# Performance work log

Measured on AMD Instinct MI355X. Metric: run time of the kernel, lower is better.

## Reference

```python
import jax, jax.numpy as jnp
import numpy as np


def softmax_one(x, axis=-1):
    # off-by-one softmax: exp(x - max) / (1 + sum(exp(x - max)))
    x = x - jnp.max(x, axis=axis, keepdims=True)
    exp_x = jnp.exp(x)
    return exp_x / (1.0 + jnp.sum(exp_x, axis=axis, keepdims=True))


def setup_inputs() -> dict:
    key = jax.random.key(0)
    kq, kk, kv = jax.random.split(key, 3)
    B, H, S, D = 2, 16, 2048, 64
    q = jax.random.normal(kq, (B, H, S, D), dtype=jnp.float32)
    k = jax.random.normal(kk, (B, H, S, D), dtype=jnp.float32)
    v = jax.random.normal(kv, (B, H, S, D), dtype=jnp.float32)
    return {"q": q, "k": k, "v": v}


def reference(q, k, v):
    d_k = k.shape[-1]
    scale = 1.0 / jnp.sqrt(jnp.asarray(d_k, dtype=q.dtype))
    # scores: [B, H, Sq, Sk]
    scores = jnp.einsum("bhqd,bhkd->bhqk", q, k) * scale
    p_attn = softmax_one(scores, axis=-1)
    # dropout p=0.0 -> identity
    out = jnp.einsum("bhqk,bhkd->bhqd", p_attn, v)
    return (out, p_attn)
```

## Files before the change

kernel.cpp:

```cpp
#include <hip/hip_runtime.h>

#define ATTN_S  2048
#define ATTN_D  64
#define ATTN_BH 32
#define QT      128
#define KT      64
#define NWAVE   8
#define LOG2E   1.4426950408889634f

typedef _Float16 half8 __attribute__((ext_vector_type(8)));
typedef _Float16 half4v __attribute__((ext_vector_type(4)));
typedef _Float16 half2v __attribute__((ext_vector_type(2)));
typedef float    floatx4 __attribute__((ext_vector_type(4)));

static __device__ __forceinline__ float fast_exp2(float x) {
#if __has_builtin(__builtin_amdgcn_exp2f)
  return __builtin_amdgcn_exp2f(x);
#else
  return exp2f(x);
#endif
}

__global__ __launch_bounds__(512)
void attn_softmax1_kernel(const float* __restrict__ Q,
                          const float* __restrict__ K,
                          const float* __restrict__ V,
                          float* __restrict__ Out,
                          float* __restrict__ P)
{
  __shared__ _Float16 sK[KT][72];
  __shared__ _Float16 sV[ATTN_D][72];
  __shared__ float    sP[NWAVE][16][68];

  const int tid  = threadIdx.x;
  const int w    = tid >> 6;
  const int lane = tid & 63;
  const int quad = lane >> 4;
  const int l15  = lane & 15;

  const int bh = blockIdx.x >> 4;
  const int q0 = (blockIdx.x & 15) * QT;

  const float* Qb = Q + (size_t)bh * ATTN_S * ATTN_D;
  const float* Kb = K + (size_t)bh * ATTN_S * ATTN_D;
  const float* Vb = V + (size_t)bh * ATTN_S * ATTN_D;
  float*       Ob = Out + (size_t)bh * ATTN_S * ATTN_D;
  float*       Pb = P + (size_t)bh * (size_t)ATTN_S * ATTN_S;

  const int qrow = q0 + w * 16 + l15;
  half8 aq[2];
  {
    const float* qr = Qb + (size_t)qrow * ATTN_D;
#pragma unroll
    for (int ch = 0; ch < 2; ++ch) {
      const floatx4* qv = (const floatx4*)(qr + ch * 32 + quad * 8);
      floatx4 f0 = qv[0], f1 = qv[1];
#pragma unroll
      for (int j = 0; j < 4; ++j) {
        aq[ch][j]     = (_Float16)(f0[j] * 0.125f);
        aq[ch][4 + j] = (_Float16)(f1[j] * 0.125f);
      }
    }
  }

  float mrow[4], lrow[4];
#pragma unroll
  for (int r = 0; r < 4; ++r) { mrow[r] = -3.0e38f; lrow[r] = 0.0f; }

#pragma unroll 1
  for (int kt = 0; kt < ATTN_S; kt += KT) {
    __syncthreads();
#pragma unroll
    for (int i = 0; i < 2; ++i) {
      int idx = tid + 512 * i;
      int r = idx >> 4, c4 = idx & 15;
      floatx4 f = *(const floatx4*)(Kb + (size_t)(kt + r) * ATTN_D + c4 * 4);
      half4v h = { (_Float16)f[0], (_Float16)f[1], (_Float16)f[2], (_Float16)f[3] };
      *(half4v*)&sK[r][c4 * 4] = h;
    }
    __syncthreads();

#pragma unroll
    for (int n = 0; n < 4; ++n) {
      half8 bk0 = *(const half8*)&sK[n * 16 + l15][quad * 8];
      half8 bk1 = *(const half8*)&sK[n * 16 + l15][32 + quad * 8];
      floatx4 acc = {0.f, 0.f, 0.f, 0.f};
      acc = __builtin_amdgcn_mfma_f32_16x16x32_f16(aq[0], bk0, acc, 0, 0, 0);
      acc = __builtin_amdgcn_mfma_f32_16x16x32_f16(aq[1], bk1, acc, 0, 0, 0);
#pragma unroll
      for (int r = 0; r < 4; ++r) {
        float s = acc[r];
        mrow[r] = fmaxf(mrow[r], s);
        lrow[r] += fast_exp2(s * LOG2E);
      }
    }
  }

  float rrow[4];
#pragma unroll
  for (int r = 0; r < 4; ++r) {
    float m = mrow[r], l = lrow[r];
#pragma unroll
    for (int off = 1; off < 16; off <<= 1) {
      m = fmaxf(m, __shfl_xor(m, off, 64));
      l += __shfl_xor(l, off, 64);
    }
    rrow[r] = 1.0f / (fast_exp2(m * LOG2E) + l);
  }

  floatx4 oacc[4];
#pragma unroll
  for (int d = 0; d < 4; ++d) oacc[d] = (floatx4){0.f, 0.f, 0.f, 0.f};

#pragma unroll 1
  for (int kt = 0; kt < ATTN_S; kt += KT) {
    __syncthreads();
#pragma unroll
    for (int i = 0; i < 2; ++i) {
      int idx = tid + 512 * i;
      int r = idx >> 4, c4 = idx & 15;
      floatx4 f = *(const floatx4*)(Kb + (size_t)(kt + r) * ATTN_D + c4 * 4);
      half4v h = { (_Float16)f[0], (_Float16)f[1], (_Float16)f[2], (_Float16)f[3] };
      *(half4v*)&sK[r][c4 * 4] = h;
    }
    {
      int rp = tid >> 4, c4 = tid & 15;
      floatx4 f0 = *(const floatx4*)(Vb + (size_t)(kt + 2 * rp) * ATTN_D + c4 * 4);
      floatx4 f1 = *(const floatx4*)(Vb + (size_t)(kt + 2 * rp + 1) * ATTN_D + c4 * 4);
#pragma unroll
      for (int c = 0; c < 4; ++c) {
        half2v h = { (_Float16)f0[c], (_Float16)f1[c] };
        *(half2v*)&sV[c4 * 4 + c][2 * rp] = h;
      }
    }
    __syncthreads();

#pragma unroll
    for (int n = 0; n < 4; ++n) {
      half8 bk0 = *(const half8*)&sK[n * 16 + l15][quad * 8];
      half8 bk1 = *(const half8*)&sK[n * 16 + l15][32 + quad * 8];
      floatx4 acc = {0.f, 0.f, 0.f, 0.f};
      acc = __builtin_amdgcn_mfma_f32_16x16x32_f16(aq[0], bk0, acc, 0, 0, 0);
      acc = __builtin_amdgcn_mfma_f32_16x16x32_f16(aq[1], bk1, acc, 0, 0, 0);
#pragma unroll
      for (int r = 0; r < 4; ++r) {
        float p = fast_exp2(acc[r] * LOG2E) * rrow[r];
        sP[w][quad * 4 + r][n * 16 + l15] = p;
      }
    }
#pragma unroll
    for (int ch = 0; ch < 2; ++ch) {
      const float* prow = &sP[w][l15][ch * 32 + quad * 8];
      half8 ap;
#pragma unroll
      for (int j = 0; j < 8; ++j) ap[j] = (_Float16)prow[j];
#pragma unroll
      for (int ds = 0; ds < 4; ++ds) {
        half8 bv = *(const half8*)&sV[ds * 16 + l15][ch * 32 + quad * 8];
        oacc[ds] = __builtin_amdgcn_mfma_f32_16x16x32_f16(ap, bv, oacc[ds], 0, 0, 0);
      }
    }
    {
      const int growbase = q0 + w * 16;
#pragma unroll
      for (int i = 0; i < 4; ++i) {
        int r = i * 4 + quad;
        floatx4 val = *(const floatx4*)&sP[w][r][l15 * 4];
        *(floatx4*)(Pb + (size_t)(growbase + r) * ATTN_S + kt + l15 * 4) = val;
      }
    }
  }

  {
    const int grow = q0 + w * 16 + quad * 4;
#pragma unroll
    for (int ds = 0; ds < 4; ++ds)
#pragma unroll
      for (int r = 0; r < 4; ++r)
        Ob[(size_t)(grow + r) * ATTN_D + ds * 16 + l15] = oacc[ds][r];
  }
}

extern "C" void kernel_launch(void* const* d_in, const int* in_sizes, int n_in,
                              void* d_out, int out_size, void* d_ws, size_t ws_size,
                              hipStream_t stream) {
  const float* Q = (const float*)d_in[0];
  const float* K = (const float*)d_in[1];
  const float* V = (const float*)d_in[2];
  float* Out = (float*)d_out;
  float* P   = Out + (size_t)ATTN_BH * ATTN_S * ATTN_D;

  dim3 grid(ATTN_BH * (ATTN_S / QT));
  dim3 block(512);
  attn_softmax1_kernel<<<grid, block, 0, stream>>>(Q, K, V, Out, P);
}
```

Before: 675.5 us.

## Preconvert Q/K/V to fp16 workspace and double-buffer tiles via direct LDS loads

A separate pre-pass converts Q (pre-scaled), K (XOR-swizzled) and V (transposed and swizzled) to fp16 in the workspace. The attention kernel then streams K/V tiles with global_load_lds into double-buffered LDS, overlapping the next tile's load with compute. It also swaps MFMA operand order so each lane holds a whole query row, which removes the shuffle reductions and lets P be written straight from registers instead of staging it through LDS. The cost is an extra kernel launch, workspace traffic, and a dependence on a large enough workspace.

Result: no change. 667.9 us (-1.1%).

```diff
diff --git a/kernel.cpp b/kernel.cpp
--- a/kernel.cpp
+++ b/kernel.cpp
@@ -1,17 +1,20 @@
 #include <hip/hip_runtime.h>
+#include <stdint.h>
 
 #define ATTN_S  2048
 #define ATTN_D  64
 #define ATTN_BH 32
 #define QT      128
 #define KT      64
+#define NT      (ATTN_S / KT)
 #define NWAVE   8
 #define LOG2E   1.4426950408889634f
 
-typedef _Float16 half8 __attribute__((ext_vector_type(8)));
-typedef _Float16 half4v __attribute__((ext_vector_type(4)));
-typedef _Float16 half2v __attribute__((ext_vector_type(2)));
+typedef _Float16 half8   __attribute__((ext_vector_type(8)));
+typedef _Float16 half4v  __attribute__((ext_vector_type(4)));
 typedef float    floatx4 __attribute__((ext_vector_type(4)));
+
+#define QH_ELEMS ((size_t)ATTN_BH * ATTN_S * ATTN_D)
 
 static __device__ __forceinline__ float fast_exp2(float x) {
 #if __has_builtin(__builtin_amdgcn_exp2f)
@@ -21,176 +24,196 @@
 #endif
 }
 
-__global__ __launch_bounds__(512)
-void attn_softmax1_kernel(const float* __restrict__ Q,
-                          const float* __restrict__ K,
-                          const float* __restrict__ V,
-                          float* __restrict__ Out,
-                          float* __restrict__ P)
+#define GLOAD16(gp, lp)                                                    \
+  __builtin_amdgcn_global_load_lds(                                        \
+      (__attribute__((address_space(1))) void*)(gp),                       \
+      (__attribute__((address_space(3))) void*)(lp), 16, 0, 0)
+
+__global__ __launch_bounds__(256)
+void preconvert_kernel(const float* __restrict__ Q, const float* __restrict__ K,
+                       const float* __restrict__ V, _Float16* __restrict__ ws)
 {
-  __shared__ _Float16 sK[KT][72];
-  __shared__ _Float16 sV[ATTN_D][72];
-  __shared__ float    sP[NWAVE][16][68];
+  if (blockIdx.x < 4096) {
+    const int gid = blockIdx.x * 256 + threadIdx.x;
+    const int isK = gid >> 19;
+    const int id  = gid & 0x7FFFF;
+    const int row = id >> 3;
+    const int c   = id & 7;
+    const float* src = (isK ? K : Q) + ((size_t)row << 6) + (c << 3);
+    floatx4 f0 = *(const floatx4*)src;
+    floatx4 f1 = *(const floatx4*)(src + 4);
+    half8 h;
+    if (!isK) {
+#pragma unroll
+      for (int j = 0; j < 4; ++j) {
+        h[j]     = (_Float16)(f0[j] * 0.125f);
+        h[4 + j] = (_Float16)(f1[j] * 0.125f);
+      }
+      *(half8*)(ws + ((size_t)row << 6) + (c << 3)) = h;
+    } else {
+#pragma unroll
+      for (int j = 0; j < 4; ++j) { h[j] = (_Float16)f0[j]; h[4 + j] = (_Float16)f1[j]; }
+      const int cp = c ^ (row & 7);
+      *(half8*)(ws + QH_ELEMS + ((size_t)row << 6) + (cp << 3)) = h;
+    }
+  } else {
+    const int blk = blockIdx.x - 4096;
+    __shared__ _Float16 sT[64][72];
+    const float* Vb = V + (size_t)blk * 64 * 64;
+#pragma unroll
+    for (int it = 0; it < 4; ++it) {
+      int lin = threadIdx.x + 256 * it;
+      int rr = lin >> 4, c4 = lin & 15;
+      floatx4 f = *(const floatx4*)(Vb + (size_t)rr * 64 + c4 * 4);
+#pragma unroll
+      for (int j = 0; j < 4; ++j) sT[rr][c4 * 4 + j] = (_Float16)f[j];
+    }
+    __syncthreads();
+    _Float16* dst = ws + 2 * QH_ELEMS + (size_t)blk * 64 * 64;
+#pragma unroll
+    for (int it = 0; it < 2; ++it) {
+      int lin = threadIdx.x + 256 * it;
+      int d = lin >> 3, cp = lin & 7;
+      int c = cp ^ (d & 7);
+      half8 h;
+#pragma unroll
+      for (int j = 0; j < 8; ++j) h[j] = sT[c * 8 + j][d];
+      *(half8*)(dst + d * 64 + cp * 8) = h;
+    }
+  }
+}
+
+__global__ __launch_bounds__(512, 4)
+void attn_softmax1_kernel(const _Float16* __restrict__ ws,
+                          float* __restrict__ Out, float* __restrict__ P)
+{
+  __shared__ __attribute__((aligned(16))) _Float16 sK [2][KT * ATTN_D];
+  __shared__ __attribute__((aligned(16))) _Float16 sVt[2][ATTN_D * KT];
+  __shared__ __attribute__((aligned(16))) _Float16 sPTh[NWAVE][16][72];
 
   const int tid  = threadIdx.x;
   const int w    = tid >> 6;
   const int lane = tid & 63;
   const int quad = lane >> 4;
   const int l15  = lane & 15;
+  const int rswz = l15 & 7;
 
   const int bh = blockIdx.x >> 4;
   const int q0 = (blockIdx.x & 15) * QT;
 
-  const float* Qb = Q + (size_t)bh * ATTN_S * ATTN_D;
-  const float* Kb = K + (size_t)bh * ATTN_S * ATTN_D;
-  const float* Vb = V + (size_t)bh * ATTN_S * ATTN_D;
-  float*       Ob = Out + (size_t)bh * ATTN_S * ATTN_D;
-  float*       Pb = P + (size_t)bh * (size_t)ATTN_S * ATTN_S;
+  const _Float16* Qh = ws + (size_t)bh * ATTN_S * ATTN_D;
+  const _Float16* Kh = ws + QH_ELEMS + (size_t)bh * ATTN_S * ATTN_D;
+  const _Float16* Vt = ws + 2 * QH_ELEMS + (size_t)bh * ATTN_S * ATTN_D;
+  float* Ob = Out + (size_t)bh * ATTN_S * ATTN_D;
+  float* Pb = P + (size_t)bh * (size_t)ATTN_S * ATTN_S;
 
   const int qrow = q0 + w * 16 + l15;
-  half8 aq[2];
-  {
-    const float* qr = Qb + (size_t)qrow * ATTN_D;
-#pragma unroll
-    for (int ch = 0; ch < 2; ++ch) {
-      const floatx4* qv = (const floatx4*)(qr + ch * 32 + quad * 8);
-      floatx4 f0 = qv[0], f1 = qv[1];
-#pragma unroll
-      for (int j = 0; j < 4; ++j) {
-        aq[ch][j]     = (_Float16)(f0[j] * 0.125f);
-        aq[ch][4 + j] = (_Float16)(f1[j] * 0.125f);
-      }
-    }
-  }
-
-  float mrow[4], lrow[4];
-#pragma unroll
-  for (int r = 0; r < 4; ++r) { mrow[r] = -3.0e38f; lrow[r] = 0.0f; }
-
-#pragma unroll 1
-  for (int kt = 0; kt < ATTN_S; kt += KT) {
-    __syncthreads();
-#pragma unroll
-    for (int i = 0; i < 2; ++i) {
-      int idx = tid + 512 * i;
-      int r = idx >> 4, c4 = idx & 15;
-      floatx4 f = *(const floatx4*)(Kb + (size_t)(kt + r) * ATTN_D + c4 * 4);
-      half4v h = { (_Float16)f[0], (_Float16)f[1], (_Float16)f[2], (_Float16)f[3] };
-      *(half4v*)&sK[r][c4 * 4] = h;
-    }
-    __syncthreads();
-
+  const half8 aq0 = *(const half8*)(Qh + (size_t)qrow * ATTN_D + quad * 8);
+  const half8 aq1 = *(const half8*)(Qh + (size_t)qrow * ATTN_D + 32 + quad * 8);
+
+  const _Float16* kg = Kh + w * (8 * ATTN_D) + lane * 8;
+  const _Float16* vg = Vt + w * (8 * KT)     + lane * 8;
+  _Float16* ldsK0 = &sK [0][w * 512];
+  _Float16* ldsK1 = &sK [1][w * 512];
+  _Float16* ldsV0 = &sVt[0][w * 512];
+  _Float16* ldsV1 = &sVt[1][w * 512];
+
+  float m4[4], l4[4];
+#pragma unroll
+  for (int r = 0; r < 4; ++r) { m4[r] = -3.0e38f; l4[r] = 0.0f; }
+
+  GLOAD16(kg, ldsK0);
+#pragma unroll 2
+  for (int t = 0; t < NT; ++t) {
+    asm volatile("s_waitcnt vmcnt(0)" ::: "memory");
+    __builtin_amdgcn_s_barrier();
+    if (t + 1 < NT) GLOAD16(kg + (size_t)(t + 1) * (KT * ATTN_D), (t & 1) ? ldsK0 : ldsK1);
+    const _Float16* kb = sK[t & 1];
 #pragma unroll
     for (int n = 0; n < 4; ++n) {
-      half8 bk0 = *(const half8*)&sK[n * 16 + l15][quad * 8];
-      half8 bk1 = *(const half8*)&sK[n * 16 + l15][32 + quad * 8];
+      half8 k0 = *(const half8*)(kb + (n * 16 + l15) * 64 + ((quad    ) ^ rswz) * 8);
+      half8 k1 = *(const half8*)(kb + (n * 16 + l15) * 64 + ((quad + 4) ^ rswz) * 8);
       floatx4 acc = {0.f, 0.f, 0.f, 0.f};
-      acc = __builtin_amdgcn_mfma_f32_16x16x32_f16(aq[0], bk0, acc, 0, 0, 0);
-      acc = __builtin_amdgcn_mfma_f32_16x16x32_f16(aq[1], bk1, acc, 0, 0, 0);
+      acc = __builtin_amdgcn_mfma_f32_16x16x32_f16(k0, aq0, acc, 0, 0, 0);
+      acc = __builtin_amdgcn_mfma_f32_16x16x32_f16(k1, aq1, acc, 0, 0, 0);
 #pragma unroll
       for (int r = 0; r < 4; ++r) {
         float s = acc[r];
-        mrow[r] = fmaxf(mrow[r], s);
-        lrow[r] += fast_exp2(s * LOG2E);
+        m4[r] = fmaxf(m4[r], s);
+        l4[r] += fast_exp2(s * LOG2E);
       }
     }
   }
-
-  float rrow[4];
-#pragma unroll
-  for (int r = 0; r < 4; ++r) {
-    float m = mrow[r], l = lrow[r];
-#pragma unroll
-    for (int off = 1; off < 16; off <<= 1) {
-      m = fmaxf(m, __shfl_xor(m, off, 64));
-      l += __shfl_xor(l, off, 64);
-    }
-    rrow[r] = 1.0f / (fast_exp2(m * LOG2E) + l);
+  float m_ = fmaxf(fmaxf(m4[0], m4[1]), fmaxf(m4[2], m4[3]));
+  float l_ = (l4[0] + l4[1]) + (l4[2] + l4[3]);
+  m_ = fmaxf(m_, __shfl_xor(m_, 16, 64));
+  l_ += __shfl_xor(l_, 16, 64);
+  m_ = fmaxf(m_, __shfl_xor(m_, 32, 64));
+  l_ += __shfl_xor(l_, 32, 64);
+  const float rinv = 1.0f / (fast_exp2(m_ * LOG2E) + l_);
+
+  floatx4 oacc[4];
+#pragma unroll
+  for (int d = 0; d < 4; ++d) oacc[d] = (floatx4){0.f, 0.f, 0.f, 0.f};
+
+  GLOAD16(kg, ldsK0);
+  GLOAD16(vg, ldsV0);
+#pragma unroll 2
+  for (int t = 0; t < NT; ++t) {
+    if (t == 0) { asm volatile("s_waitcnt vmcnt(0)" ::: "memory"); }
+    else        { asm volatile("s_waitcnt vmcnt(4)" ::: "memory"); }
+    __builtin_amdgcn_s_barrier();
+    if (t + 1 < NT) {
+      GLOAD16(kg + (size_t)(t + 1) * (KT * ATTN_D), (t & 1) ? ldsK0 : ldsK1);
+      GLOAD16(vg + (size_t)(t + 1) * (ATTN_D * KT), (t & 1) ? ldsV0 : ldsV1);
+    }
+    const _Float16* kb = sK [t & 1];
+    const _Float16* vb = sVt[t & 1];
+    const int kbase = t * KT;
+
+#pragma unroll
+    for (int n = 0; n < 4; ++n) {
+      half8 k0 = *(const half8*)(kb + (n * 16 + l15) * 64 + ((quad    ) ^ rswz) * 8);
+      half8 k1 = *(const half8*)(kb + (n * 16 + l15) * 64 + ((quad + 4) ^ rswz) * 8);
+      floatx4 acc = {0.f, 0.f, 0.f, 0.f};
+      acc = __builtin_amdgcn_mfma_f32_16x16x32_f16(k0, aq0, acc, 0, 0, 0);
+      acc = __builtin_amdgcn_mfma_f32_16x16x32_f16(k1, aq1, acc, 0, 0, 0);
+      floatx4 pv;
+#pragma unroll
+      for (int r = 0; r < 4; ++r) pv[r] = fast_exp2(acc[r] * LOG2E) * rinv;
+      *(floatx4*)(Pb + (size_t)qrow * ATTN_S + kbase + n * 16 + quad * 4) = pv;
+      half4v hp = { (_Float16)pv[0], (_Float16)pv[1], (_Float16)pv[2], (_Float16)pv[3] };
+      *(half4v*)&sPTh[w][l15][n * 16 + quad * 4] = hp;
+    }
+#pragma unroll
+    for (int ch = 0; ch < 2; ++ch) {
+      half8 bp = *(const half8*)&sPTh[w][l15][ch * 32 + quad * 8];
+#pragma unroll
+      for (int dt = 0; dt < 4; ++dt) {
+        half8 av = *(const half8*)(vb + (dt * 16 + l15) * 64 + ((ch * 4 + quad) ^ rswz) * 8);
+        oacc[dt] = __builtin_amdgcn_mfma_f32_16x16x32_f16(av, bp, oacc[dt], 0, 0, 0);
+      }
+    }
   }
 
-  floatx4 oacc[4];
-#pragma unroll
-  for (int d = 0; d < 4; ++d) oacc[d] = (floatx4){0.f, 0.f, 0.f, 0.f};
-
-#pragma unroll 1
-  for (int kt = 0; kt < ATTN_S; kt += KT) {
-    __syncthreads();
-#pragma unroll
-    for (int i = 0; i < 2; ++i) {
-      int idx = tid + 512 * i;
-      int r = idx >> 4, c4 = idx & 15;
-      floatx4 f = *(const floatx4*)(Kb + (size_t)(kt + r) * ATTN_D + c4 * 4);
-      half4v h = { (_Float16)f[0], (_Float16)f[1], (_Float16)f[2], (_Float16)f[3] };
-      *(half4v*)&sK[r][c4 * 4] = h;
-    }
-    {
-      int rp = tid >> 4, c4 = tid & 15;
-      floatx4 f0 = *(const floatx4*)(Vb + (size_t)(kt + 2 * rp) * ATTN_D + c4 * 4);
-      floatx4 f1 = *(const floatx4*)(Vb + (size_t)(kt + 2 * rp + 1) * ATTN_D + c4 * 4);
-#pragma unroll
-      for (int c = 0; c < 4; ++c) {
-        half2v h = { (_Float16)f0[c], (_Float16)f1[c] };
-        *(half2v*)&sV[c4 * 4 + c][2 * rp] = h;
-      }
-    }
-    __syncthreads();
-
-#pragma unroll
-    for (int n = 0; n < 4; ++n) {
-      half8 bk0 = *(const half8*)&sK[n * 16 + l15][quad * 8];
-      half8 bk1 = *(const half8*)&sK[n * 16 + l15][32 + quad * 8];
-      floatx4 acc = {0.f, 0.f, 0.f, 0.f};
-      acc = __builtin_amdgcn_mfma_f32_16x16x32_f16(aq[0], bk0, acc, 0, 0, 0);
-      acc = __builtin_amdgcn_mfma_f32_16x16x32_f16(aq[1], bk1, acc, 0, 0, 0);
-#pragma unroll
-      for (int r = 0; r < 4; ++r) {
-        float p = fast_exp2(acc[r] * LOG2E) * rrow[r];
-        sP[w][quad * 4 + r][n * 16 + l15] = p;
-      }
-    }
-#pragma unroll
-    for (int ch = 0; ch < 2; ++ch) {
-      const float* prow = &sP[w][l15][ch * 32 + quad * 8];
-      half8 ap;
-#pragma unroll
-      for (int j = 0; j < 8; ++j) ap[j] = (_Float16)prow[j];
-#pragma unroll
-      for (int ds = 0; ds < 4; ++ds) {
-        half8 bv = *(const half8*)&sV[ds * 16 + l15][ch * 32 + quad * 8];
-        oacc[ds] = __builtin_amdgcn_mfma_f32_16x16x32_f16(ap, bv, oacc[ds], 0, 0, 0);
-      }
-    }
-    {
-      const int growbase = q0 + w * 16;
-#pragma unroll
-      for (int i = 0; i < 4; ++i) {
-        int r = i * 4 + quad;
-        floatx4 val = *(const floatx4*)&sP[w][r][l15 * 4];
-        *(floatx4*)(Pb + (size_t)(growbase + r) * ATTN_S + kt + l15 * 4) = val;
-      }
-    }
-  }
-
-  {
-    const int grow = q0 + w * 16 + quad * 4;
-#pragma unroll
-    for (int ds = 0; ds < 4; ++ds)
-#pragma unroll
-      for (int r = 0; r < 4; ++r)
-        Ob[(size_t)(grow + r) * ATTN_D + ds * 16 + l15] = oacc[ds][r];
-  }
+#pragma unroll
+  for (int dt = 0; dt < 4; ++dt)
+#pragma unroll
+    for (int r = 0; r < 4; ++r)
+      Ob[(size_t)qrow * ATTN_D + dt * 16 + quad * 4 + r] = oacc[dt][r];
 }
 
 extern "C" void kernel_launch(void* const* d_in, const int* in_sizes, int n_in,
                               void* d_out, int out_size, void* d_ws, size_t ws_size,
                               hipStream_t stream) {
+  (void)in_sizes; (void)n_in; (void)out_size; (void)ws_size;
   const float* Q = (const float*)d_in[0];
   const float* K = (const float*)d_in[1];
   const float* V = (const float*)d_in[2];
   float* Out = (float*)d_out;
   float* P   = Out + (size_t)ATTN_BH * ATTN_S * ATTN_D;
-
-  dim3 grid(ATTN_BH * (ATTN_S / QT));
-  dim3 block(512);
-  attn_softmax1_kernel<<<grid, block, 0, stream>>>(Q, K, V, Out, P);
-}
+  _Float16* ws = (_Float16*)d_ws;
+
+  preconvert_kernel<<<dim3(4096 + 1024), dim3(256), 0, stream>>>(Q, K, V, ws);
+  attn_softmax1_kernel<<<dim3(ATTN_BH * (ATTN_S / QT)), dim3(512), 0, stream>>>(ws, Out, P);
+}
```
